# Optimization experiments

Hardware: AMD Instinct MI355X
Metric: run time of the kernel (lower is better)

## Reference

```python
import jax, jax.numpy as jnp
import numpy as np

H, C = 4, 32            # heads, per-head channels
HID = H * C             # 128
IN_DIM, OUT_DIM = 300, 4
N, E = 50000, 800000
TE = HID // H           # time-encode dim = 32
EDGE_DIM = 2 * TE + 3   # 67
L = 2                   # num_layers


def setup_inputs() -> dict:
    key = jax.random.key(0)
    ks = jax.random.split(key, 20)
    p = lambda k, shape: jax.random.normal(k, shape, jnp.float32) * 0.02
    return {
        "x": jax.random.normal(ks[0], (N, IN_DIM), jnp.float32),
        "ei_td": jax.random.randint(ks[1], (2, E), 0, N),
        "ei_bu": jax.random.randint(ks[2], (2, E), 0, N),
        "ea_td": jax.random.uniform(ks[3], (E, 4), jnp.float32),
        "ea_bu": jax.random.uniform(ks[4], (E, 4), jnp.float32),
        "W_in": p(ks[5], (IN_DIM, HID)), "b_in": jnp.zeros((HID,), jnp.float32),
        "te_w": jax.random.uniform(ks[6], (TE,), jnp.float32),
        # stacked TransformerConv params: [layer, etype(TD,BU), ...]
        "Wq": p(ks[7], (L, 2, HID, HID)), "bq": jnp.zeros((L, 2, HID), jnp.float32),
        "Wk": p(ks[8], (L, 2, HID, HID)), "bk": jnp.zeros((L, 2, HID), jnp.float32),
        "Wv": p(ks[9], (L, 2, HID, HID)), "bv": jnp.zeros((L, 2, HID), jnp.float32),
        "We": p(ks[10], (L, 2, EDGE_DIM, HID)),  # lin_edge has no bias in PyG
        "Wskip": p(ks[11], (L, 2, HID, HID)), "bskip": jnp.zeros((L, 2, HID), jnp.float32),
        "gamma": jnp.ones((L, HID), jnp.float32), "beta": jnp.zeros((L, HID), jnp.float32),
        "W_out": p(ks[12], ((L + 1) * HID, OUT_DIM)), "b_out": jnp.zeros((OUT_DIM,), jnp.float32),
        "W_dec": p(ks[13], (HID, IN_DIM)), "b_dec": jnp.zeros((IN_DIM,), jnp.float32),
    }


def _edge_enc(ea, te_w):
    # TimeEncode on dt_norm, then [sin, cos, w_norm, infl_flag, cos_sim]
    ft = ea[:, 1:2] * te_w  # [E, TE]
    return jnp.concatenate([jnp.sin(ft), jnp.cos(ft), ea[:, 0:1], ea[:, 2:3], ea[:, 3:4]], axis=1)


def _tconv(h, src, dst, enc, Wq, bq, Wk, bk, Wv, bv, We, Wskip, bskip):
    # PyG TransformerConv (concat=True, root_weight=True, beta=False)
    n = h.shape[0]
    q = (h @ Wq + bq).reshape(n, H, C)
    k = (h @ Wk + bk).reshape(n, H, C)
    v = (h @ Wv + bv).reshape(n, H, C)
    e = (enc @ We).reshape(-1, H, C)                 # per-edge key/value offset
    ke = k[src] + e                                  # [E,H,C]
    alpha = jnp.einsum('ehc,ehc->eh', q[dst], ke) / jnp.sqrt(jnp.float32(C))
    amax = jax.ops.segment_max(alpha, dst, num_segments=n)     # scatter-softmax
    ex = jnp.exp(alpha - amax[dst])
    den = jax.ops.segment_sum(ex, dst, num_segments=n)
    a = ex / (den[dst] + 1e-16)                      # [E,H]
    msg = (v[src] + e) * a[:, :, None]
    out = jax.ops.segment_sum(msg, dst, num_segments=n).reshape(n, HID)
    return out + h @ Wskip + bskip                   # root/skip connection


def _ln(x, g, b):
    mu = jnp.mean(x, axis=-1, keepdims=True)
    var = jnp.mean((x - mu) ** 2, axis=-1, keepdims=True)
    return (x - mu) / jnp.sqrt(var + 1e-5) * g + b


def reference(x, ei_td, ei_bu, ea_td, ea_bu, W_in, b_in, te_w,
              Wq, bq, Wk, bk, Wv, bv, We, Wskip, bskip,
              gamma, beta, W_out, b_out, W_dec, b_dec):
    h = jax.nn.relu(x @ W_in + b_in)
    outs = [h]
    enc_td = _edge_enc(ea_td, te_w)
    enc_bu = _edge_enc(ea_bu, te_w)
    for i in range(L):
        o_td = _tconv(h, ei_td[0], ei_td[1], enc_td,
                      Wq[i, 0], bq[i, 0], Wk[i, 0], bk[i, 0], Wv[i, 0], bv[i, 0],
                      We[i, 0], Wskip[i, 0], bskip[i, 0])
        o_bu = _tconv(h, ei_bu[0], ei_bu[1], enc_bu,
                      Wq[i, 1], bq[i, 1], Wk[i, 1], bk[i, 1], Wv[i, 1], bv[i, 1],
                      We[i, 1], Wskip[i, 1], bskip[i, 1])
        t = jax.nn.relu(o_td + o_bu)                 # HeteroConv aggr='sum'; dropout=eval noop
        h = _ln(t, gamma[i], beta[i])
        outs.append(h)
    out = jnp.concatenate(outs, axis=1) @ W_out + b_out   # JumpingKnowledge 'cat'
    z = outs[-1]
    x_rec = z @ W_dec + b_dec
    return (out, z, x_rec)
```

## Files before the change

### kernel.cpp

```cpp
#include <hip/hip_runtime.h>

#define HID 128
#define CH 32
#define DPAD 68
#define PSTR 272
#define INDIM 300
#define QROW 384

typedef __attribute__((ext_vector_type(8))) short short8v;
typedef __attribute__((ext_vector_type(4))) short short4v;
typedef __attribute__((ext_vector_type(4))) float float4v;

__device__ __forceinline__ unsigned bf16_rne(float f){
  unsigned u = __float_as_uint(f);
  return (u + 0x7fffu + ((u >> 16) & 1u)) >> 16;
}
__device__ __forceinline__ void split_bf16(float f, short& hi, short& lo){
  unsigned h = bf16_rne(f);
  float fh = __uint_as_float(h << 16);
  unsigned l = bf16_rne(f - fh);
  hi = (short)h; lo = (short)l;
}
__device__ __forceinline__ float b2f(short s){
  return __uint_as_float(((unsigned)(unsigned short)s) << 16);
}
__device__ __forceinline__ int invperm32(int s31){
  return ((s31 >> 2) & 1) * 16 + ((s31 >> 3) & 3) * 4 + (s31 & 3);
}

__global__ void k_hist(const int* __restrict__ ei, int E, int* __restrict__ deg){
  int i = blockIdx.x*256 + threadIdx.x;
  if(i < E) atomicAdd(&deg[ei[E + i]], 1);
}

__global__ void k_scan(const int* __restrict__ deg, int n, int* __restrict__ seg, int* __restrict__ cur){
  __shared__ int wsum[16];
  __shared__ int wpre[16];
  int t = threadIdx.x;
  int wv = t >> 6, ln = t & 63;
  int running = 0;
  for(int base = 0; base < n; base += 8192){
    int vloc[8]; int idx0 = base + t*8;
    int s8 = 0;
    #pragma unroll
    for(int j=0;j<8;j++){ int ii = idx0+j; int d = (ii<n)? deg[ii] : 0; vloc[j] = s8; s8 += d; }
    int inc = s8;
    #pragma unroll
    for(int off=1; off<64; off<<=1){
      int y = __shfl_up(inc, off, 64);
      if (ln >= off) inc += y;
    }
    if (ln == 63) wsum[wv] = inc;
    __syncthreads();
    if (t < 16){
      int v = wsum[t];
      #pragma unroll
      for(int off=1; off<16; off<<=1){
        int y = __shfl_up(v, off, 64);
        if (t >= off) v += y;
      }
      wpre[t] = v;
    }
    __syncthreads();
    int wbase = (wv==0) ? 0 : wpre[wv-1];
    int excl = wbase + inc - s8;
    #pragma unroll
    for(int j=0;j<8;j++){
      int ii = idx0+j;
      if(ii<n){ int val = running + excl + vloc[j]; seg[ii]=val; cur[ii]=val; }
    }
    int total = wpre[15];
    __syncthreads();
    running += total;
  }
  if (t==0) seg[n] = running;
}

__global__ void k_scatter(const int* __restrict__ ei, const float* __restrict__ ea, int E,
                          int* __restrict__ cur, int* __restrict__ srcs, float4* __restrict__ eas){
  int i = blockIdx.x*256 + threadIdx.x;
  if(i >= E) return;
  int d = ei[E + i];
  int pos = atomicAdd(&cur[d], 1);
  srcs[pos] = ei[i];
  eas[pos] = ((const float4*)ea)[i];
}

__global__ void k_split(const float* __restrict__ W, short* __restrict__ bh, short* __restrict__ bl,
                        int K, int N, int Kpad, int Npad){
  int idx = blockIdx.x*256 + threadIdx.x;
  if (idx >= Npad*Kpad) return;
  int n = idx / Kpad, s = idx - n*Kpad;
  int k = (s & ~31) + invperm32(s & 31);
  float v = (n < N && k < K) ? W[(size_t)k*N + n] : 0.f;
  short hi, lo; split_bf16(v, hi, lo);
  bh[idx] = hi; bl[idx] = lo;
}

__global__ void k_split4(const float* __restrict__ W0, const float* __restrict__ W1,
                         const float* __restrict__ W2, const float* __restrict__ W3,
                         short* __restrict__ bh, short* __restrict__ bl){
  int slab = blockIdx.y;
  const float* W = (slab==0)?W0:(slab==1)?W1:(slab==2)?W2:W3;
  int idx = blockIdx.x*256 + threadIdx.x;
  int n = idx >> 7, s = idx & 127;
  int k = (s & ~31) + invperm32(s & 31);
  float v = W[k*HID + n];
  short hi, lo; split_bf16(v, hi, lo);
  bh[slab*16384 + idx] = hi; bl[slab*16384 + idx] = lo;
}

__global__ void k_wqwe_s(const float* __restrict__ Wq, const float* __restrict__ We,
                         short* __restrict__ bh, short* __restrict__ bl){
  int idx = blockIdx.x*256 + threadIdx.x;
  if (idx >= 384*128) return;
  int n = idx >> 7, s = idx & 127;
  int k = (s & ~31) + invperm32(s & 31);
  float v = 0.f;
  if (n < PSTR){
    int h = n / DPAD, d = n - h*DPAD;
    if (d < 67){
      const float* wr = Wq + k*HID + h*CH;
      const float* er = We + d*HID + h*CH;
      #pragma unroll
      for(int c=0;c<CH;c++) v += wr[c]*er[c];
    }
  }
  short hi, lo; split_bf16(v, hi, lo);
  bh[idx]=hi; bl[idx]=lo;
}

__global__ void k_pbias(const float* __restrict__ bq, const float* __restrict__ We, float* __restrict__ pbv){
  int n = blockIdx.x*256 + threadIdx.x;
  if (n >= PSTR) return;
  int h = n / DPAD, d = n - h*DPAD;
  float v = 0.f;
  if (d < 67){
    #pragma unroll
    for(int c=0;c<CH;c++) v += bq[h*CH+c]*We[d*HID + h*CH + c];
  }
  pbv[n] = v;
}

__global__ void k_weexp_s(const float* __restrict__ We, short* __restrict__ bh, short* __restrict__ bl){
  int idx = blockIdx.x*256 + threadIdx.x;
  if (idx >= 128*320) return;
  int n = idx / 320, s = idx - n*320;
  int k = (s & ~31) + invperm32(s & 31);
  float v = 0.f;
  if (k < PSTR){
    int h = k / DPAD, d = k - h*DPAD;
    if (d < 67 && (n>>5)==h) v = We[d*HID + n];
  }
  short hi, lo; split_bf16(v, hi, lo);
  bh[idx]=hi; bl[idx]=lo;
}

__global__ void k_bias4(const float* __restrict__ b0, const float* __restrict__ b1,
                        const float* __restrict__ b2, const float* __restrict__ b3,
                        float* __restrict__ out){
  int t = blockIdx.x*256 + threadIdx.x;
  if (t >= 512) return;
  float v = (t<128)? b0[t] : (t<256)? b1[t-128] : (t<384)? b2[t-256] : b3[t-384];
  out[t] = v;
}

__global__ void k_splitA(const float* __restrict__ A, short* __restrict__ ah, short* __restrict__ al, int total){
  int i = blockIdx.x*256 + threadIdx.x;
  if (i >= total) return;
  short hi, lo; split_bf16(A[i], hi, lo);
  ah[i]=hi; al[i]=lo;
}

__global__ __launch_bounds__(256,2) void k_gemm(
        const short* __restrict__ Ah, const short* __restrict__ Al, const float* __restrict__ Af,
        const short* __restrict__ Bh, const short* __restrict__ Bl,
        const float* __restrict__ bias, float* __restrict__ C,
        short* __restrict__ Ch, short* __restrict__ Cl,
        int M, int N, int K, int Ks, int Kpad, int mode){
  __shared__ short Ash[64*64], Asl[64*64];
  __shared__ short Bsh[128*64], Bsl[128*64];
  int tid = threadIdx.x;
  int l = tid & 63, w = tid >> 6;
  int lr = l & 15, q = l >> 4;
  int row0 = blockIdx.x*64, col0 = blockIdx.y*128;
  float4v acc[4][2];
  #pragma unroll
  for(int mt=0;mt<4;mt++){
    #pragma unroll
    for(int nt=0;nt<2;nt++) acc[mt][nt] = (float4v){0.f,0.f,0.f,0.f};
  }
  for (int k0 = 0; k0 < Kpad; k0 += 64){
    if (Af){
      #pragma unroll
      for (int i=0;i<4;i++){
        int c = tid + i*256;
        int row = c >> 4, kq = c & 15;
        int gr = row0 + row, gk = k0 + kq*4;
        float4 a4 = make_float4(0.f,0.f,0.f,0.f);
        if (gr < M && gk < K) a4 = *(const float4*)(Af + (size_t)gr*Ks + gk);
        short h0,h1,h2,h3,l0,l1,l2,l3;
        split_bf16(a4.x,h0,l0); split_bf16(a4.y,h1,l1);
        split_bf16(a4.z,h2,l2); split_bf16(a4.w,h3,l3);
        int cb = ((kq>>3)*64 + (kq&3)*16 + ((kq>>2)&1)*8) ^ ((row&7)<<4);
        int ih = row*64 + (cb>>1);
        *(short4v*)&Ash[ih] = (short4v){h0,h1,h2,h3};
        *(short4v*)&Asl[ih] = (short4v){l0,l1,l2,l3};
      }
    } else {
      #pragma unroll
      for (int i=0;i<4;i++){
        int c = tid + i*256;
        int row = c >> 4, kq = c & 15;
        int gr = row0 + row, gk = k0 + kq*4;
        short4v a4h = (short4v){0,0,0,0}, a4l = (short4v){0,0,0,0};
        if (gr < M && gk < K){
          a4h = *(const short4v*)(Ah + (size_t)gr*Ks + gk);
          a4l = *(const short4v*)(Al + (size_t)gr*Ks + gk);
        }
        int cb = ((kq>>3)*64 + (kq&3)*16 + ((kq>>2)&1)*8) ^ ((row&7)<<4);
        int ih = row*64 + (cb>>1);
        *(short4v*)&Ash[ih] = a4h;
        *(short4v*)&Asl[ih] = a4l;
      }
    }
    #pragma unroll
    for (int i=0;i<4;i++){
      int c = tid + i*256;
      int n = c >> 3, c8 = c & 7;
      size_t gidx = (size_t)(col0 + n)*Kpad + k0 + c8*8;
      int cb = (c8*16) ^ ((n&7)<<4);
      int ih = n*64 + (cb>>1);
      *(short8v*)&Bsh[ih] = *(const short8v*)(Bh + gidx);
      *(short8v*)&Bsl[ih] = *(const short8v*)(Bl + gidx);
    }
    __syncthreads();
    #pragma unroll
    for (int ks=0; ks<2; ks++){
      short8v ah[4], al[4], bh[2], bl[2];
      #pragma unroll
      for (int mt=0; mt<4; mt++){
        int r = mt*16 + lr;
        int cb = (ks*64 + q*16) ^ ((r&7)<<4);
        int ih = r*64 + (cb>>1);
        ah[mt] = *(const short8v*)&Ash[ih];
        al[mt] = *(const short8v*)&Asl[ih];
      }
      #pragma unroll
      for (int nt=0; nt<2; nt++){
        int r = w*32 + nt*16 + lr;
        int cb = (ks*64 + q*16) ^ ((r&7)<<4);
        int ih = r*64 + (cb>>1);
        bh[nt] = *(const short8v*)&Bsh[ih];
        bl[nt] = *(const short8v*)&Bsl[ih];
      }
      #pragma unroll
      for (int mt=0; mt<4; mt++){
        #pragma unroll
        for (int nt=0; nt<2; nt++){
          acc[mt][nt] = __builtin_amdgcn_mfma_f32_16x16x32_bf16(ah[mt], bh[nt], acc[mt][nt], 0,0,0);
          acc[mt][nt] = __builtin_amdgcn_mfma_f32_16x16x32_bf16(ah[mt], bl[nt], acc[mt][nt], 0,0,0);
          acc[mt][nt] = __builtin_amdgcn_mfma_f32_16x16x32_bf16(al[mt], bh[nt], acc[mt][nt], 0,0,0);
        }
      }
    }
    __syncthreads();
  }
  short* qs = (short*)C;
  #pragma unroll
  for (int mt=0; mt<4; mt++){
    #pragma unroll
    for (int nt=0; nt<2; nt++){
      int gc = col0 + w*32 + nt*16 + lr;
      if (mode != 3 && gc >= N) continue;
      float bv = bias ? bias[gc] : 0.f;
      #pragma unroll
      for (int r=0; r<4; r++){
        int gr = row0 + mt*16 + q*4 + r;
        if (gr >= M) continue;
        float v = acc[mt][nt][r] + bv;
        if (mode == 3){
          if (gc < 256) C[(size_t)gr*QROW + gc] = v;
          else          qs[(size_t)gr*(QROW*2) + 256 + gc] = (short)bf16_rne(v);
        } else if (mode == 4){
          v = fmaxf(v, 0.f);
          short hi, lo; split_bf16(v, hi, lo);
          Ch[(size_t)gr*N + gc] = hi;
          Cl[(size_t)gr*N + gc] = lo;
        } else {
          float* cp = C + (size_t)gr*N + gc;
          if (mode == 2) v += *cp;
          *cp = v;
        }
      }
    }
  }
}

__global__ __launch_bounds__(256) void k_attn(const float* __restrict__ qkvs, const float* __restrict__ P,
      const int* __restrict__ srcs, const float4* __restrict__ eas,
      const int* __restrict__ seg, const float* __restrict__ tw,
      float* __restrict__ acc, float* __restrict__ S, int Nn, int addmode){
  int tid = threadIdx.x;
  int wid = (blockIdx.x * 256 + tid) >> 6;
  int lane = tid & 63;
  if(wid >= Nn) return;
  int beg = seg[wid], end = seg[wid+1];
  int g = lane >> 4, l = lane & 15;
  int hown = l >> 2;
  const float* rowq = qkvs + (size_t)wid*QROW;
  float4 qa = *(const float4*)(rowq + l*8), qb4 = *(const float4*)(rowq + l*8 + 4);
  float qv[8] = {qa.x,qa.y,qa.z,qa.w,qb4.x,qb4.y,qb4.z,qb4.w};
  float Pr[4][4], Pt[4];
  #pragma unroll
  for(int h=0;h<4;h++){
    float4 pv = *(const float4*)(P + (size_t)wid*PSTR + h*DPAD + l*4);
    Pr[h][0]=pv.x; Pr[h][1]=pv.y; Pr[h][2]=pv.z; Pr[h][3]=pv.w;
    Pt[h] = (l<4) ? P[(size_t)wid*PSTR + h*DPAD + 64 + l] : 0.f;
  }
  float twv[4];
  #pragma unroll
  for(int t=0;t<4;t++) twv[t] = tw[((l&7)<<2) + t];
  bool issin = (l < 8);
  float mx[4] = {-3.0e38f,-3.0e38f,-3.0e38f,-3.0e38f};
  float den[4] = {0.f,0.f,0.f,0.f};
  float accv[8] = {0.f,0.f,0.f,0.f,0.f,0.f,0.f,0.f};
  float accS[4][4] = {{0.f}};
  float accT[4] = {0.f,0.f,0.f,0.f};
  for(int e0 = beg; e0 < end; e0 += 4){
    int e = e0 + g;
    if(e < end){
      int src = srcs[e];
      const short* kvp = (const short*)(qkvs + (size_t)src*QROW) + 512 + l*8;
      short8v k8 = *(const short8v*)kvp;
      short8v v8 = *(const short8v*)(kvp + 128);
      float qk = 0.f;
      #pragma unroll
      for(int j=0;j<8;j++) qk += qv[j]*b2f(k8[j]);
      float p[4] = {0.f,0.f,0.f,0.f};
      p[hown] = qk;
      float4 ea4 = eas[e];
      float ea1 = ea4.y;
      float ec[4];
      #pragma unroll
      for(int t=0;t<4;t++){
        float ft = ea1 * twv[t];
        ec[t] = issin ? __sinf(ft) : __cosf(ft);
      }
      #pragma unroll
      for(int h=0;h<4;h++){
        #pragma unroll
        for(int t=0;t<4;t++) p[h] += ec[t]*Pr[h][t];
      }
      float et = 0.f;
      if(l < 4){
        et = (l==0)? ea4.x : (l==1)? ea4.z : (l==2)? ea4.w : 0.f;
        #pragma unroll
        for(int h=0;h<4;h++) p[h] += et*Pt[h];
      }
      #pragma unroll
      for(int m=1;m<16;m<<=1){
        #pragma unroll
        for(int h=0;h<4;h++) p[h] += __shfl_xor(p[h], m, 64);
      }
      float eh[4], fs[4];
      #pragma unroll
      for(int h=0;h<4;h++){
        float a = p[h]*0.17677669529663687f;
        float nm = fmaxf(mx[h], a);
        fs[h] = __expf(mx[h] - nm);
        eh[h] = __expf(a - nm);
        den[h] = den[h]*fs[h] + eh[h];
        mx[h] = nm;
      }
      float fo = fs[hown], eo = eh[hown];
      #pragma unroll
      for(int j=0;j<8;j++) accv[j] = accv[j]*fo + eo*b2f(v8[j]);
      #pragma unroll
      for(int h=0;h<4;h++){
        #pragma unroll
        for(int t=0;t<4;t++) accS[h][t] = accS[h][t]*fs[h] + eh[h]*ec[t];
      }
      if(l < 4){
        #pragma unroll
        for(int h=0;h<4;h++) accT[h] = accT[h]*fs[h] + eh[h]*et;
      }
    }
  }
  float gm[4], cf[4];
  #pragma unroll
  for(int h=0;h<4;h++) gm[h] = mx[h];
  #pragma unroll
  for(int m=16;m<64;m<<=1){
    #pragma unroll
    for(int h=0;h<4;h++) gm[h] = fmaxf(gm[h], __shfl_xor(gm[h], m, 64));
  }
  #pragma unroll
  for(int h=0;h<4;h++){
    cf[h] = __expf(mx[h] - gm[h]);
    den[h] *= cf[h];
  }
  float co = cf[hown];
  #pragma unroll
  for(int j=0;j<8;j++) accv[j] *= co;
  #pragma unroll
  for(int h=0;h<4;h++){
    #pragma unroll
    for(int t=0;t<4;t++) accS[h][t] *= cf[h];
    accT[h] *= cf[h];
  }
  #pragma unroll
  for(int m=16;m<64;m<<=1){
    #pragma unroll
    for(int h=0;h<4;h++) den[h] += __shfl_xor(den[h], m, 64);
    #pragma unroll
    for(int j=0;j<8;j++) accv[j] += __shfl_xor(accv[j], m, 64);
    #pragma unroll
    for(int h=0;h<4;h++){
      #pragma unroll
      for(int t=0;t<4;t++) accS[h][t] += __shfl_xor(accS[h][t], m, 64);
      accT[h] += __shfl_xor(accT[h], m, 64);
    }
  }
  float rden[4];
  #pragma unroll
  for(int h=0;h<4;h++) rden[h] = 1.f / (den[h] + 1e-16f);
  if(g == 0){
    float ro = rden[hown];
    float4 s0 = *(const float4*)(rowq + 128 + l*8);
    float4 s1 = *(const float4*)(rowq + 128 + l*8 + 4);
    float o[8];
    o[0]=accv[0]*ro+s0.x; o[1]=accv[1]*ro+s0.y; o[2]=accv[2]*ro+s0.z; o[3]=accv[3]*ro+s0.w;
    o[4]=accv[4]*ro+s1.x; o[5]=accv[5]*ro+s1.y; o[6]=accv[6]*ro+s1.z; o[7]=accv[7]*ro+s1.w;
    float* op = acc + (size_t)wid*HID + l*8;
    if (addmode){
      float4 a0 = *(const float4*)op, a1 = *(const float4*)(op+4);
      o[0]+=a0.x; o[1]+=a0.y; o[2]+=a0.z; o[3]+=a0.w;
      o[4]+=a1.x; o[5]+=a1.y; o[6]+=a1.z; o[7]+=a1.w;
    }
    *(float4*)op     = make_float4(o[0],o[1],o[2],o[3]);
    *(float4*)(op+4) = make_float4(o[4],o[5],o[6],o[7]);
    #pragma unroll
    for(int h=0;h<4;h++){
      *(float4*)(S + (size_t)wid*PSTR + h*DPAD + l*4) =
          make_float4(accS[h][0]*rden[h],accS[h][1]*rden[h],accS[h][2]*rden[h],accS[h][3]*rden[h]);
    }
    if(l < 4){
      #pragma unroll
      for(int h=0;h<4;h++) S[(size_t)wid*PSTR + h*DPAD + 64 + l] = accT[h]*rden[h];
    }
  }
}

__global__ __launch_bounds__(256) void k_ln(const float* __restrict__ acc,
   const float* __restrict__ gamma, const float* __restrict__ beta,
   float* __restrict__ hout, short* __restrict__ Hh, short* __restrict__ Hl, int Nn){
  int wid = (blockIdx.x*blockDim.x + threadIdx.x) >> 6;
  int lane = threadIdx.x & 63;
  if(wid >= Nn) return;
  size_t b = (size_t)wid*HID;
  int c0 = lane, c1 = lane + 64;
  float t0 = fmaxf(acc[b+c0], 0.f);
  float t1 = fmaxf(acc[b+c1], 0.f);
  float s = t0+t1, ss = t0*t0+t1*t1;
  #pragma unroll
  for(int m=1;m<64;m<<=1){ s += __shfl_xor(s,m,64); ss += __shfl_xor(ss,m,64); }
  float mu = s * (1.f/128.f);
  float var = ss*(1.f/128.f) - mu*mu;
  float rstd = 1.f / sqrtf(var + 1e-5f);
  float y0 = (t0-mu)*rstd*gamma[c0] + beta[c0];
  float y1 = (t1-mu)*rstd*gamma[c1] + beta[c1];
  hout[b+c0] = y0; hout[b+c1] = y1;
  short h0,l0,h1,l1;
  split_bf16(y0,h0,l0); split_bf16(y1,h1,l1);
  Hh[b+c0]=h0; Hl[b+c0]=l0;
  Hh[b+c1]=h1; Hl[b+c1]=l1;
}

__global__ __launch_bounds__(256) void k_out4(const short* __restrict__ H0h, const short* __restrict__ H0l,
    const short* __restrict__ H1h, const short* __restrict__ H1l, const float* __restrict__ z,
    const float* __restrict__ Wout, const float* __restrict__ bout,
    float* __restrict__ out, int Nn){
  __shared__ float Wl[384*4];
  int tid = threadIdx.x;
  #pragma unroll
  for(int i=0;i<6;i++) Wl[tid + i*256] = Wout[tid + i*256];
  __syncthreads();
  int wid = (blockIdx.x*256 + tid) >> 6;
  int lane = tid & 63;
  if(wid >= Nn) return;
  float p0=0.f,p1=0.f,p2=0.f,p3=0.f;
  #pragma unroll
  for(int ch=0; ch<6; ch++){
    int kidx = ch*64 + lane;
    float x;
    if (kidx < 128){
      size_t ix = (size_t)wid*HID + kidx;
      x = b2f(H0h[ix]) + b2f(H0l[ix]);
    } else if (kidx < 256){
      size_t ix = (size_t)wid*HID + (kidx-128);
      x = b2f(H1h[ix]) + b2f(H1l[ix]);
    } else {
      x = z[(size_t)wid*HID + (kidx-256)];
    }
    float4 w4 = *(const float4*)&Wl[kidx*4];
    p0 += x*w4.x; p1 += x*w4.y; p2 += x*w4.z; p3 += x*w4.w;
  }
  #pragma unroll
  for(int m=1;m<64;m<<=1){
    p0 += __shfl_xor(p0,m,64); p1 += __shfl_xor(p1,m,64);
    p2 += __shfl_xor(p2,m,64); p3 += __shfl_xor(p3,m,64);
  }
  if(lane < 4){
    float pv = (lane==0)?p0:(lane==1)?p1:(lane==2)?p2:p3;
    out[(size_t)wid*4 + lane] = pv + bout[lane];
  }
}

extern "C" void kernel_launch(void* const* d_in, const int* in_sizes, int n_in,
                              void* d_out, int out_size, void* d_ws, size_t ws_size,
                              hipStream_t stream) {
  const float* x    = (const float*)d_in[0];
  const int*   ei_td= (const int*)d_in[1];
  const int*   ei_bu= (const int*)d_in[2];
  const float* ea_td= (const float*)d_in[3];
  const float* ea_bu= (const float*)d_in[4];
  const float* W_in = (const float*)d_in[5];
  const float* b_in = (const float*)d_in[6];
  const float* te_w = (const float*)d_in[7];
  const float* Wq   = (const float*)d_in[8];
  const float* bq   = (const float*)d_in[9];
  const float* Wk   = (const float*)d_in[10];
  const float* bk   = (const float*)d_in[11];
  const float* Wv   = (const float*)d_in[12];
  const float* bv   = (const float*)d_in[13];
  const float* We   = (const float*)d_in[14];
  const float* Wsk  = (const float*)d_in[15];
  const float* bsk  = (const float*)d_in[16];
  const float* gamma= (const float*)d_in[17];
  const float* beta = (const float*)d_in[18];
  const float* Wout = (const float*)d_in[19];
  const float* bout = (const float*)d_in[20];
  const float* Wdec = (const float*)d_in[21];
  const float* bdec = (const float*)d_in[22];
  (void)n_in; (void)out_size; (void)ws_size;

  int Nn = in_sizes[0] / INDIM;
  int Et = in_sizes[1] / 2;
  int Eb = in_sizes[2] / 2;

  float* outF = (float*)d_out;
  float* z_reg    = outF + (size_t)Nn*4;
  float* xrec_reg = z_reg + (size_t)Nn*HID;
  float* accb = z_reg;
  float* Pbuf = xrec_reg;
  float* tail = xrec_reg + (size_t)Nn*PSTR;
  int* seg_td = (int*)tail;      tail += Nn+1;
  int* seg_bu = (int*)tail;      tail += Nn+1;
  int* cur    = (int*)tail;      tail += Nn;
  int* deg    = (int*)tail;      tail += Nn;

  char* p = (char*)d_ws;
  auto alloc = [&](size_t bytes)->void*{ void* r = (void*)p; p += (bytes + 255) & ~(size_t)255; return r; };
  float* qkvs  = (float*)alloc((size_t)Nn*QROW*4);
  short* H0h   = (short*)alloc((size_t)Nn*HID*2);
  short* H0l   = (short*)alloc((size_t)Nn*HID*2);
  short* H1h   = (short*)alloc((size_t)Nn*HID*2);
  short* H1l   = (short*)alloc((size_t)Nn*HID*2);
  int* srcs_td = (int*)alloc((size_t)Et*4);
  int* srcs_bu = (int*)alloc((size_t)Eb*4);
  float* eas_td= (float*)alloc((size_t)Et*4*4);
  float* eas_bu= (float*)alloc((size_t)Eb*4*4);
  short* btQ_h = (short*)alloc(65536*2);
  short* btQ_l = (short*)alloc(65536*2);
  short* btP_h = (short*)alloc(49152*2);
  short* btP_l = (short*)alloc(49152*2);
  short* btE_h = (short*)alloc(40960*2);
  short* btE_l = (short*)alloc(40960*2);
  short* btG_h = (short*)alloc(49152*2);
  short* btG_l = (short*)alloc(49152*2);
  float* qbias = (float*)alloc(512*4);
  float* pbv   = (float*)alloc(PSTR*4);
  short* xh = (short*)qkvs;
  short* xl = xh + (size_t)Nn*INDIM;
  short* Zh = (short*)qkvs;
  short* Zl = Zh + (size_t)Nn*HID;

  hipMemsetAsync(deg, 0, (size_t)Nn*4, stream);
  k_hist<<<(Et+255)/256, 256, 0, stream>>>(ei_td, Et, deg);
  k_scan<<<1, 1024, 0, stream>>>(deg, Nn, seg_td, cur);
  k_scatter<<<(Et+255)/256, 256, 0, stream>>>(ei_td, ea_td, Et, cur, srcs_td, (float4*)eas_td);

  hipMemsetAsync(deg, 0, (size_t)Nn*4, stream);
  k_hist<<<(Eb+255)/256, 256, 0, stream>>>(ei_bu, Eb, deg);
  k_scan<<<1, 1024, 0, stream>>>(deg, Nn, seg_bu, cur);
  k_scatter<<<(Eb+255)/256, 256, 0, stream>>>(ei_bu, ea_bu, Eb, cur, srcs_bu, (float4*)eas_bu);

  int gM = (Nn + 63) / 64;
  k_splitA<<<((Nn*INDIM)+255)/256, 256, 0, stream>>>(x, xh, xl, Nn*INDIM);
  k_split<<<(128*320+255)/256, 256, 0, stream>>>(W_in, btG_h, btG_l, INDIM, HID, 320, 128);
  k_gemm<<<dim3(gM,1), 256, 0, stream>>>(xh, xl, nullptr, btG_h, btG_l, b_in,
        nullptr, H0h, H0l, Nn, HID, INDIM, INDIM, 320, 4);

  for(int i = 0; i < 2; i++){
    const short* Hh = (i==0)? H0h : H1h;
    const short* Hl = (i==0)? H0l : H1l;
    for(int et = 0; et < 2; et++){
      int wi = i*2 + et;
      const float* Wq_ = Wq + (size_t)wi*HID*HID; const float* bq_ = bq + (size_t)wi*HID;
      const float* Wk_ = Wk + (size_t)wi*HID*HID; const float* bk_ = bk + (size_t)wi*HID;
      const float* Wv_ = Wv + (size_t)wi*HID*HID; const float* bv_ = bv + (size_t)wi*HID;
      const float* Ws_ = Wsk+ (size_t)wi*HID*HID; const float* bs_ = bsk+ (size_t)wi*HID;
      const float* We_ = We + (size_t)wi*67*HID;
      const int* seg  = et ? seg_bu : seg_td;
      const int* srcs = et ? srcs_bu : srcs_td;
      const float* eas= et ? eas_bu : eas_td;

      k_split4<<<dim3(64,4), 256, 0, stream>>>(Wq_, Ws_, Wk_, Wv_, btQ_h, btQ_l);
      k_bias4<<<2, 256, 0, stream>>>(bq_, bs_, bk_, bv_, qbias);
      k_wqwe_s<<<192, 256, 0, stream>>>(Wq_, We_, btP_h, btP_l);
      k_pbias<<<2, 256, 0, stream>>>(bq_, We_, pbv);
      k_weexp_s<<<160, 256, 0, stream>>>(We_, btE_h, btE_l);

      k_gemm<<<dim3(gM,4), 256, 0, stream>>>(Hh, Hl, nullptr, btQ_h, btQ_l, qbias,
            qkvs, nullptr, nullptr, Nn, 512, HID, HID, HID, 3);
      k_gemm<<<dim3(gM,3), 256, 0, stream>>>(Hh, Hl, nullptr, btP_h, btP_l, pbv,
            Pbuf, nullptr, nullptr, Nn, PSTR, HID, HID, HID, 0);
      k_attn<<<(Nn*64+255)/256, 256, 0, stream>>>(qkvs, Pbuf, srcs, (const float4*)eas,
                                                  seg, te_w, accb, Pbuf, Nn, et);
      k_gemm<<<dim3(gM,1), 256, 0, stream>>>(nullptr, nullptr, Pbuf, btE_h, btE_l, nullptr,
            accb, nullptr, nullptr, Nn, HID, PSTR, PSTR, 320, 2);
    }
    if (i == 0)
      k_ln<<<(Nn*64+255)/256, 256, 0, stream>>>(accb, gamma, beta, z_reg, H1h, H1l, Nn);
    else
      k_ln<<<(Nn*64+255)/256, 256, 0, stream>>>(accb, gamma + HID, beta + HID, z_reg, Zh, Zl, Nn);
  }

  k_out4<<<(Nn*64+255)/256, 256, 0, stream>>>(H0h, H0l, H1h, H1l, z_reg, Wout, bout, outF, Nn);
  k_split<<<(384*128+255)/256, 256, 0, stream>>>(Wdec, btG_h, btG_l, HID, INDIM, 128, 384);
  k_gemm<<<dim3(gM,3), 256, 0, stream>>>(Zh, Zl, nullptr, btG_h, btG_l, bdec,
        xrec_reg, nullptr, nullptr, Nn, INDIM, HID, HID, 128, 0);
}
```

Baseline: 1.969 ms.

## Fuse QKV and P projections, enlarge GEMM tiles, drop softmax max tracking

```diff
diff --git a/kernel.cpp b/kernel.cpp
--- a/kernel.cpp
+++ b/kernel.cpp
@@ -130,16 +130,18 @@
   bh[idx]=hi; bl[idx]=lo;
 }
 
-__global__ void k_pbias(const float* __restrict__ bq, const float* __restrict__ We, float* __restrict__ pbv){
+__global__ void k_pbias(const float* __restrict__ bq, const float* __restrict__ We, float* __restrict__ out){
   int n = blockIdx.x*256 + threadIdx.x;
-  if (n >= PSTR) return;
-  int h = n / DPAD, d = n - h*DPAD;
+  if (n >= 384) return;
   float v = 0.f;
-  if (d < 67){
-    #pragma unroll
-    for(int c=0;c<CH;c++) v += bq[h*CH+c]*We[d*HID + h*CH + c];
-  }
-  pbv[n] = v;
+  if (n < PSTR){
+    int h = n / DPAD, d = n - h*DPAD;
+    if (d < 67){
+      #pragma unroll
+      for(int c=0;c<CH;c++) v += bq[h*CH+c]*We[d*HID + h*CH + c];
+    }
+  }
+  out[n] = v;
 }
 
 __global__ void k_weexp_s(const float* __restrict__ We, short* __restrict__ bh, short* __restrict__ bl){
@@ -165,36 +167,30 @@
   out[t] = v;
 }
 
-__global__ void k_splitA(const float* __restrict__ A, short* __restrict__ ah, short* __restrict__ al, int total){
-  int i = blockIdx.x*256 + threadIdx.x;
-  if (i >= total) return;
-  short hi, lo; split_bf16(A[i], hi, lo);
-  ah[i]=hi; al[i]=lo;
-}
-
-__global__ __launch_bounds__(256,2) void k_gemm(
+__global__ __launch_bounds__(512,4) void k_gemm(
         const short* __restrict__ Ah, const short* __restrict__ Al, const float* __restrict__ Af,
         const short* __restrict__ Bh, const short* __restrict__ Bl,
         const float* __restrict__ bias, float* __restrict__ C,
-        short* __restrict__ Ch, short* __restrict__ Cl,
+        short* __restrict__ Ch, short* __restrict__ Cl, float* __restrict__ Pout,
         int M, int N, int K, int Ks, int Kpad, int mode){
-  __shared__ short Ash[64*64], Asl[64*64];
+  __shared__ short Ash[128*64], Asl[128*64];
   __shared__ short Bsh[128*64], Bsl[128*64];
   int tid = threadIdx.x;
   int l = tid & 63, w = tid >> 6;
   int lr = l & 15, q = l >> 4;
-  int row0 = blockIdx.x*64, col0 = blockIdx.y*128;
-  float4v acc[4][2];
-  #pragma unroll
-  for(int mt=0;mt<4;mt++){
-    #pragma unroll
-    for(int nt=0;nt<2;nt++) acc[mt][nt] = (float4v){0.f,0.f,0.f,0.f};
+  int wr = w >> 1, wc = w & 1;
+  int row0 = blockIdx.x*128, col0 = blockIdx.y*128;
+  float4v acc[2][4];
+  #pragma unroll
+  for(int mt=0;mt<2;mt++){
+    #pragma unroll
+    for(int nt=0;nt<4;nt++) acc[mt][nt] = (float4v){0.f,0.f,0.f,0.f};
   }
   for (int k0 = 0; k0 < Kpad; k0 += 64){
     if (Af){
       #pragma unroll
       for (int i=0;i<4;i++){
-        int c = tid + i*256;
+        int c = tid + i*512;
         int row = c >> 4, kq = c & 15;
         int gr = row0 + row, gk = k0 + kq*4;
         float4 a4 = make_float4(0.f,0.f,0.f,0.f);
@@ -210,7 +206,7 @@
     } else {
       #pragma unroll
       for (int i=0;i<4;i++){
-        int c = tid + i*256;
+        int c = tid + i*512;
         int row = c >> 4, kq = c & 15;
         int gr = row0 + row, gk = k0 + kq*4;
         short4v a4h = (short4v){0,0,0,0}, a4l = (short4v){0,0,0,0};
@@ -225,8 +221,8 @@
       }
     }
     #pragma unroll
-    for (int i=0;i<4;i++){
-      int c = tid + i*256;
+    for (int i=0;i<2;i++){
+      int c = tid + i*512;
       int n = c >> 3, c8 = c & 7;
       size_t gidx = (size_t)(col0 + n)*Kpad + k0 + c8*8;
       int cb = (c8*16) ^ ((n&7)<<4);
@@ -237,27 +233,27 @@
     __syncthreads();
     #pragma unroll
     for (int ks=0; ks<2; ks++){
-      short8v ah[4], al[4], bh[2], bl[2];
-      #pragma unroll
-      for (int mt=0; mt<4; mt++){
-        int r = mt*16 + lr;
+      short8v ah[2], al[2], bh[4], bl[4];
+      #pragma unroll
+      for (int mt=0; mt<2; mt++){
+        int r = wr*32 + mt*16 + lr;
         int cb = (ks*64 + q*16) ^ ((r&7)<<4);
         int ih = r*64 + (cb>>1);
         ah[mt] = *(const short8v*)&Ash[ih];
         al[mt] = *(const short8v*)&Asl[ih];
       }
       #pragma unroll
-      for (int nt=0; nt<2; nt++){
-        int r = w*32 + nt*16 + lr;
+      for (int nt=0; nt<4; nt++){
+        int r = wc*64 + nt*16 + lr;
         int cb = (ks*64 + q*16) ^ ((r&7)<<4);
         int ih = r*64 + (cb>>1);
         bh[nt] = *(const short8v*)&Bsh[ih];
         bl[nt] = *(const short8v*)&Bsl[ih];
       }
       #pragma unroll
-      for (int mt=0; mt<4; mt++){
+      for (int mt=0; mt<2; mt++){
         #pragma unroll
-        for (int nt=0; nt<2; nt++){
+        for (int nt=0; nt<4; nt++){
           acc[mt][nt] = __builtin_amdgcn_mfma_f32_16x16x32_bf16(ah[mt], bh[nt], acc[mt][nt], 0,0,0);
           acc[mt][nt] = __builtin_amdgcn_mfma_f32_16x16x32_bf16(ah[mt], bl[nt], acc[mt][nt], 0,0,0);
           acc[mt][nt] = __builtin_amdgcn_mfma_f32_16x16x32_bf16(al[mt], bh[nt], acc[mt][nt], 0,0,0);
@@ -268,20 +264,21 @@
   }
   short* qs = (short*)C;
   #pragma unroll
-  for (int mt=0; mt<4; mt++){
-    #pragma unroll
-    for (int nt=0; nt<2; nt++){
-      int gc = col0 + w*32 + nt*16 + lr;
-      if (mode != 3 && gc >= N) continue;
+  for (int mt=0; mt<2; mt++){
+    #pragma unroll
+    for (int nt=0; nt<4; nt++){
+      int gc = col0 + wc*64 + nt*16 + lr;
+      if (gc >= N) continue;
       float bv = bias ? bias[gc] : 0.f;
       #pragma unroll
       for (int r=0; r<4; r++){
-        int gr = row0 + mt*16 + q*4 + r;
+        int gr = row0 + wr*32 + mt*16 + q*4 + r;
         if (gr >= M) continue;
         float v = acc[mt][nt][r] + bv;
         if (mode == 3){
-          if (gc < 256) C[(size_t)gr*QROW + gc] = v;
-          else          qs[(size_t)gr*(QROW*2) + 256 + gc] = (short)bf16_rne(v);
+          if (gc < 256)      C[(size_t)gr*QROW + gc] = v;
+          else if (gc < 512) qs[(size_t)gr*(QROW*2) + 256 + gc] = (short)bf16_rne(v);
+          else { int pc = gc - 512; if (pc < PSTR) Pout[(size_t)gr*PSTR + pc] = v; }
         } else if (mode == 4){
           v = fmaxf(v, 0.f);
           short hi, lo; split_bf16(v, hi, lo);
@@ -322,7 +319,6 @@
   #pragma unroll
   for(int t=0;t<4;t++) twv[t] = tw[((l&7)<<2) + t];
   bool issin = (l < 8);
-  float mx[4] = {-3.0e38f,-3.0e38f,-3.0e38f,-3.0e38f};
   float den[4] = {0.f,0.f,0.f,0.f};
   float accv[8] = {0.f,0.f,0.f,0.f,0.f,0.f,0.f,0.f};
   float accS[4][4] = {{0.f}};
@@ -363,51 +359,25 @@
         #pragma unroll
         for(int h=0;h<4;h++) p[h] += __shfl_xor(p[h], m, 64);
       }
-      float eh[4], fs[4];
+      float eh[4];
       #pragma unroll
       for(int h=0;h<4;h++){
-        float a = p[h]*0.17677669529663687f;
-        float nm = fmaxf(mx[h], a);
-        fs[h] = __expf(mx[h] - nm);
-        eh[h] = __expf(a - nm);
-        den[h] = den[h]*fs[h] + eh[h];
-        mx[h] = nm;
-      }
-      float fo = fs[hown], eo = eh[hown];
-      #pragma unroll
-      for(int j=0;j<8;j++) accv[j] = accv[j]*fo + eo*b2f(v8[j]);
+        eh[h] = __expf(p[h]*0.17677669529663687f);
+        den[h] += eh[h];
+      }
+      float eo = eh[hown];
+      #pragma unroll
+      for(int j=0;j<8;j++) accv[j] += eo*b2f(v8[j]);
       #pragma unroll
       for(int h=0;h<4;h++){
         #pragma unroll
-        for(int t=0;t<4;t++) accS[h][t] = accS[h][t]*fs[h] + eh[h]*ec[t];
+        for(int t=0;t<4;t++) accS[h][t] += eh[h]*ec[t];
       }
       if(l < 4){
         #pragma unroll
-        for(int h=0;h<4;h++) accT[h] = accT[h]*fs[h] + eh[h]*et;
-      }
-    }
-  }
-  float gm[4], cf[4];
-  #pragma unroll
-  for(int h=0;h<4;h++) gm[h] = mx[h];
-  #pragma unroll
-  for(int m=16;m<64;m<<=1){
-    #pragma unroll
-    for(int h=0;h<4;h++) gm[h] = fmaxf(gm[h], __shfl_xor(gm[h], m, 64));
-  }
-  #pragma unroll
-  for(int h=0;h<4;h++){
-    cf[h] = __expf(mx[h] - gm[h]);
-    den[h] *= cf[h];
-  }
-  float co = cf[hown];
-  #pragma unroll
-  for(int j=0;j<8;j++) accv[j] *= co;
-  #pragma unroll
-  for(int h=0;h<4;h++){
-    #pragma unroll
-    for(int t=0;t<4;t++) accS[h][t] *= cf[h];
-    accT[h] *= cf[h];
+        for(int h=0;h<4;h++) accT[h] += eh[h]*et;
+      }
+    }
   }
   #pragma unroll
   for(int m=16;m<64;m<<=1){
@@ -571,18 +541,13 @@
   int* srcs_bu = (int*)alloc((size_t)Eb*4);
   float* eas_td= (float*)alloc((size_t)Et*4*4);
   float* eas_bu= (float*)alloc((size_t)Eb*4*4);
-  short* btQ_h = (short*)alloc(65536*2);
-  short* btQ_l = (short*)alloc(65536*2);
-  short* btP_h = (short*)alloc(49152*2);
-  short* btP_l = (short*)alloc(49152*2);
+  short* btQP_h= (short*)alloc((size_t)896*128*2);
+  short* btQP_l= (short*)alloc((size_t)896*128*2);
   short* btE_h = (short*)alloc(40960*2);
   short* btE_l = (short*)alloc(40960*2);
   short* btG_h = (short*)alloc(49152*2);
   short* btG_l = (short*)alloc(49152*2);
-  float* qbias = (float*)alloc(512*4);
-  float* pbv   = (float*)alloc(PSTR*4);
-  short* xh = (short*)qkvs;
-  short* xl = xh + (size_t)Nn*INDIM;
+  float* qbias = (float*)alloc(896*4);
   short* Zh = (short*)qkvs;
   short* Zl = Zh + (size_t)Nn*HID;
 
@@ -596,11 +561,10 @@
   k_scan<<<1, 1024, 0, stream>>>(deg, Nn, seg_bu, cur);
   k_scatter<<<(Eb+255)/256, 256, 0, stream>>>(ei_bu, ea_bu, Eb, cur, srcs_bu, (float4*)eas_bu);
 
-  int gM = (Nn + 63) / 64;
-  k_splitA<<<((Nn*INDIM)+255)/256, 256, 0, stream>>>(x, xh, xl, Nn*INDIM);
+  int gM = (Nn + 127) / 128;
   k_split<<<(128*320+255)/256, 256, 0, stream>>>(W_in, btG_h, btG_l, INDIM, HID, 320, 128);
-  k_gemm<<<dim3(gM,1), 256, 0, stream>>>(xh, xl, nullptr, btG_h, btG_l, b_in,
-        nullptr, H0h, H0l, Nn, HID, INDIM, INDIM, 320, 4);
+  k_gemm<<<dim3(gM,1), 512, 0, stream>>>(nullptr, nullptr, x, btG_h, btG_l, b_in,
+        nullptr, H0h, H0l, nullptr, Nn, HID, INDIM, INDIM, 320, 4);
 
   for(int i = 0; i < 2; i++){
     const short* Hh = (i==0)? H0h : H1h;
@@ -616,20 +580,18 @@
       const int* srcs = et ? srcs_bu : srcs_td;
       const float* eas= et ? eas_bu : eas_td;
 
-      k_split4<<<dim3(64,4), 256, 0, stream>>>(Wq_, Ws_, Wk_, Wv_, btQ_h, btQ_l);
+      k_split4<<<dim3(64,4), 256, 0, stream>>>(Wq_, Ws_, Wk_, Wv_, btQP_h, btQP_l);
       k_bias4<<<2, 256, 0, stream>>>(bq_, bs_, bk_, bv_, qbias);
-      k_wqwe_s<<<192, 256, 0, stream>>>(Wq_, We_, btP_h, btP_l);
-      k_pbias<<<2, 256, 0, stream>>>(bq_, We_, pbv);
+      k_wqwe_s<<<192, 256, 0, stream>>>(Wq_, We_, btQP_h + 512*128, btQP_l + 512*128);
+      k_pbias<<<2, 256, 0, stream>>>(bq_, We_, qbias + 512);
       k_weexp_s<<<160, 256, 0, stream>>>(We_, btE_h, btE_l);
 
-      k_gemm<<<dim3(gM,4), 256, 0, stream>>>(Hh, Hl, nullptr, btQ_h, btQ_l, qbias,
-            qkvs, nullptr, nullptr, Nn, 512, HID, HID, HID, 3);
-      k_gemm<<<dim3(gM,3), 256, 0, stream>>>(Hh, Hl, nullptr, btP_h, btP_l, pbv,
-            Pbuf, nullptr, nullptr, Nn, PSTR, HID, HID, HID, 0);
+      k_gemm<<<dim3(gM,7), 512, 0, stream>>>(Hh, Hl, nullptr, btQP_h, btQP_l, qbias,
+            qkvs, nullptr, nullptr, Pbuf, Nn, 896, HID, HID, HID, 3);
       k_attn<<<(Nn*64+255)/256, 256, 0, stream>>>(qkvs, Pbuf, srcs, (const float4*)eas,
                                                   seg, te_w, accb, Pbuf, Nn, et);
-      k_gemm<<<dim3(gM,1), 256, 0, stream>>>(nullptr, nullptr, Pbuf, btE_h, btE_l, nullptr,
-            accb, nullptr, nullptr, Nn, HID, PSTR, PSTR, 320, 2);
+      k_gemm<<<dim3(gM,1), 512, 0, stream>>>(nullptr, nullptr, Pbuf, btE_h, btE_l, nullptr,
+            accb, nullptr, nullptr, nullptr, Nn, HID, PSTR, PSTR, 320, 2);
     }
     if (i == 0)
       k_ln<<<(Nn*64+255)/256, 256, 0, stream>>>(accb, gamma, beta, z_reg, H1h, H1l, Nn);
@@ -639,6 +601,6 @@
 
   k_out4<<<(Nn*64+255)/256, 256, 0, stream>>>(H0h, H0l, H1h, H1l, z_reg, Wout, bout, outF, Nn);
   k_split<<<(384*128+255)/256, 256, 0, stream>>>(Wdec, btG_h, btG_l, HID, INDIM, 128, 384);
-  k_gemm<<<dim3(gM,3), 256, 0, stream>>>(Zh, Zl, nullptr, btG_h, btG_l, bdec,
-        xrec_reg, nullptr, nullptr, Nn, INDIM, HID, HID, 128, 0);
-}
+  k_gemm<<<dim3(gM,3), 512, 0, stream>>>(Zh, Zl, nullptr, btG_h, btG_l, bdec,
+        xrec_reg, nullptr, nullptr, nullptr, Nn, INDIM, HID, HID, 128, 0);
+}
```

New measurement: 1.716 ms. 1.15x faster.
